# Kernel tuning notes

Hardware: AMD Instinct MI355X
Metric: run time of the kernel (lower is better)

Reference implementation:

```python
import jax, jax.numpy as jnp
import numpy as np

N, E = 100000, 1600000
D_IN, D_H, D_OUT = 128, 128, 64


def setup_inputs() -> dict:
    key = jax.random.key(0)
    ks = jax.random.split(key, 9)
    features = jax.random.normal(ks[0], (N, D_IN), dtype=jnp.float32)
    src = jax.random.randint(ks[1], (E,), 0, N, dtype=jnp.int32)
    dst = jax.random.randint(ks[2], (E,), 0, N, dtype=jnp.int32)
    # GraphConv weights (glorot-ish scale)
    W1 = jax.random.normal(ks[3], (D_IN, D_H), dtype=jnp.float32) * (1.0 / np.sqrt(D_IN))
    b1 = jnp.zeros((D_H,), dtype=jnp.float32)
    W2 = jax.random.normal(ks[4], (D_H, D_H), dtype=jnp.float32) * (1.0 / np.sqrt(D_H))
    b2 = jnp.zeros((D_H,), dtype=jnp.float32)
    W3 = jax.random.normal(ks[5], (D_H, D_OUT), dtype=jnp.float32) * (1.0 / np.sqrt(D_H))
    b3 = jnp.zeros((D_OUT,), dtype=jnp.float32)
    return {"features": features, "src": src, "dst": dst,
            "W1": W1, "b1": b1, "W2": W2, "b2": b2, "W3": W3, "b3": b3}


def reference(features, src, dst, W1, b1, W2, b2, W3, b3):
    n = features.shape[0]
    ones_e = jnp.ones(src.shape[0], dtype=features.dtype)
    # DGL GraphConv norm='both': degrees clamped to min 1
    out_deg = jnp.clip(jax.ops.segment_sum(ones_e, src, num_segments=n), 1.0)
    in_deg = jnp.clip(jax.ops.segment_sum(ones_e, dst, num_segments=n), 1.0)
    norm_src = out_deg ** -0.5  # [N]
    norm_dst = in_deg ** -0.5   # [N]

    def graph_conv(h, W, b, relu):
        h = h * norm_src[:, None]                                   # D_out^{-1/2} scale
        m = jax.ops.segment_sum(h[src], dst, num_segments=n)        # SpMM aggregate
        m = m * norm_dst[:, None]                                   # D_in^{-1/2} scale
        h = m @ W + b                                               # linear
        return jax.nn.relu(h) if relu else h

    # dropout is identity in eval mode (deterministic reference)
    h = graph_conv(features, W1, b1, True)
    h = graph_conv(h, W2, b2, True)
    h = graph_conv(h, W3, b3, False)
    return jax.nn.log_softmax(h, axis=1)
```

## Files before the change

### kernel.cpp

```cpp
#include <hip/hip_runtime.h>
#include <math.h>

#define D 128
#define DO 64

#define CHUNK_BITS 15
#define CHUNK_SZ   32768
#define HWORDS     (CHUNK_SZ/4)
#define NSLICE     64

typedef unsigned int uint32;
typedef short bf8s __attribute__((ext_vector_type(8)));
typedef float f32x16 __attribute__((ext_vector_type(16)));

__device__ __forceinline__ unsigned short f2bf(float f) {
    uint32 u = __float_as_uint(f);
    u += 0x7FFFu + ((u >> 16) & 1u);
    return (unsigned short)(u >> 16);
}
__device__ __forceinline__ float bf_lo(uint32 p) { return __uint_as_float(p << 16); }
__device__ __forceinline__ float bf_hi(uint32 p) { return __uint_as_float(p & 0xFFFF0000u); }
__device__ __forceinline__ void acc2(float4& a, uint2 q) {
    a.x += bf_lo(q.x); a.y += bf_hi(q.x);
    a.z += bf_lo(q.y); a.w += bf_hi(q.y);
}

__device__ __forceinline__ f32x16 mfma32(bf8s a, bf8s b, f32x16 c) {
    return __builtin_amdgcn_mfma_f32_32x32x16_bf16(a, b, c, 0, 0, 0);
}
#define ZERO16 {0.f,0.f,0.f,0.f,0.f,0.f,0.f,0.f,0.f,0.f,0.f,0.f,0.f,0.f,0.f,0.f}

__global__ void k_pack_w(const float* __restrict__ W1, const float* __restrict__ W2,
                         const float* __restrict__ W3,
                         unsigned short* __restrict__ P1, unsigned short* __restrict__ P2,
                         unsigned short* __restrict__ P3) {
    int t = blockIdx.x * 256 + threadIdx.x;
    const float* W; unsigned short* P; int slot, NCT, ncols;
    if (t < 2048)      { W = W1; P = P1; slot = t;        NCT = 4; ncols = 128; }
    else if (t < 4096) { W = W2; P = P2; slot = t - 2048; NCT = 4; ncols = 128; }
    else if (t < 5120) { W = W3; P = P3; slot = t - 4096; NCT = 2; ncols = 64;  }
    else return;
    int lane = slot & 63, rest = slot >> 6;
    int ct = rest % NCT, ks = rest / NCT;
    int k0 = ks * 16 + (lane >> 5) * 8;
    int colidx = ct * 32 + (lane & 31);
    unsigned u[4];
#pragma unroll
    for (int b = 0; b < 4; ++b) {
        unsigned lo = f2bf(W[(size_t)(k0 + 2 * b) * ncols + colidx]);
        unsigned hi = f2bf(W[(size_t)(k0 + 2 * b + 1) * ncols + colidx]);
        u[b] = lo | (hi << 16);
    }
    ((uint4*)P)[slot] = make_uint4(u[0], u[1], u[2], u[3]);
}

__global__ __launch_bounds__(256) void k_hist_gemm1(
    const int* __restrict__ src, const int* __restrict__ dst, int E,
    int NH, int NBg, int gemmPer,
    uint32* __restrict__ histS, uint32* __restrict__ histD,
    const float* __restrict__ F, const unsigned short* __restrict__ Wp1,
    unsigned short* __restrict__ T1, int N) {
    __shared__ __align__(16) char smemraw[64 * 132 * 4];
    const int tid = threadIdx.x;
    const int P = 1 + gemmPer;
    const int per = blockIdx.x / P;
    const int pos = blockIdx.x % P;

    if (pos == 0) {
        if (per >= 2 * NH) return;
        bool isS = per >= NH;
        int h = isS ? per - NH : per;
        int chunk = h / NSLICE, slice = h % NSLICE;
        const int* key = isS ? src : dst;
        uint32* hist = (uint32*)smemraw;
        for (int w = tid; w < HWORDS; w += 256) hist[w] = 0;
        __syncthreads();
        int base = chunk << CHUNK_BITS;
        const int nE4 = E >> 2;
        int lo = (int)(((long long)slice * nE4) / NSLICE);
        int hi = (int)(((long long)(slice + 1) * nE4) / NSLICE);
        for (int idx = lo + tid; idx < hi; idx += 256) {
            int4 k4 = ((const int4*)key)[idx];
            unsigned o;
            o = (unsigned)(k4.x - base); if (o < CHUNK_SZ) atomicAdd(&hist[o >> 2], 1u << ((o & 3) * 8));
            o = (unsigned)(k4.y - base); if (o < CHUNK_SZ) atomicAdd(&hist[o >> 2], 1u << ((o & 3) * 8));
            o = (unsigned)(k4.z - base); if (o < CHUNK_SZ) atomicAdd(&hist[o >> 2], 1u << ((o & 3) * 8));
            o = (unsigned)(k4.w - base); if (o < CHUNK_SZ) atomicAdd(&hist[o >> 2], 1u << ((o & 3) * 8));
        }
        if (slice == NSLICE - 1 && tid == 0) {
            for (int i = nE4 * 4; i < E; ++i) {
                unsigned o = (unsigned)(key[i] - base);
                if (o < CHUNK_SZ) atomicAdd(&hist[o >> 2], 1u << ((o & 3) * 8));
            }
        }
        __syncthreads();
        uint32* outp = (isS ? histS : histD) + (size_t)h * HWORDS;
        for (int w = tid; w < HWORDS; w += 256) outp[w] = hist[w];
        return;
    }
    int gid = per * gemmPer + (pos - 1);
    if (gid >= NBg) return;
    const int n0 = gid * 64;
    const float4* M4 = (const float4*)F;
#pragma unroll
    for (int it = 0; it < 8; ++it) {
        int id = it * 256 + tid;
        int nl = id >> 5, k4 = id & 31;
        float4 v = make_float4(0.f, 0.f, 0.f, 0.f);
        int n = n0 + nl;
        if (n < N) v = M4[(size_t)n * 32 + k4];
        ushort4 o;
        o.x = f2bf(v.x); o.y = f2bf(v.y); o.z = f2bf(v.z); o.w = f2bf(v.w);
        *(ushort4*)(smemraw + ((unsigned)(nl * 256 + k4 * 8) ^ ((nl & 15) << 4))) = o;
    }
    __syncthreads();
    const int wid = tid >> 6, wl = tid & 63;
    const int rt = wid >> 1, ctb = (wid & 1) * 2;
    const bf8s* Wp = (const bf8s*)Wp1;
    f32x16 acc0 = ZERO16, acc1 = ZERO16;
    const int arow = rt * 32 + (wl & 31);
    const unsigned axor = (unsigned)((arow & 15) << 4);
    const unsigned abase = (unsigned)(arow * 256 + (wl >> 5) * 16);
#pragma unroll
    for (int ks = 0; ks < 8; ++ks) {
        bf8s af = *(const bf8s*)(smemraw + ((abase + ks * 32) ^ axor));
        acc0 = mfma32(af, Wp[(ks * 4 + ctb) * 64 + wl], acc0);
        acc1 = mfma32(af, Wp[(ks * 4 + ctb + 1) * 64 + wl], acc1);
    }
    const int colb = wl & 31;
    const int rbase = rt * 32 + ((wl >> 5) << 2);
#pragma unroll
    for (int reg = 0; reg < 16; ++reg) {
        int n = n0 + (reg & 3) + 8 * (reg >> 2) + rbase;
        if (n < N) {
            T1[(size_t)n * 128 + ctb * 32 + colb] = f2bf(acc0[reg]);
            T1[(size_t)n * 128 + (ctb + 1) * 32 + colb] = f2bf(acc1[reg]);
        }
    }
}

__global__ void k_merge_norms(const uint32* __restrict__ histS, uint32* __restrict__ histD,
                              int* __restrict__ degi, float* __restrict__ ns,
                              float* __restrict__ nd, int N, int NCHUNK) {
    int w = blockIdx.x * 256 + threadIdx.x;
    if (w >= NCHUNK * HWORDS) return;
    int chunk = w / HWORDS, ww = w - chunk * HWORDS;
    int n0 = (chunk << CHUNK_BITS) + ww * 4;
    if (n0 >= N) return;
    size_t basehist = ((size_t)chunk * NSLICE) * HWORDS + ww;
    uint32 runD = 0, runS = 0;
#pragma unroll 4
    for (int s = 0; s < NSLICE; ++s) {
        size_t idx = basehist + (size_t)s * HWORDS;
        uint32 c = histD[idx];
        histD[idx] = runD;
        runD += c;
        runS += histS[idx];
    }
#pragma unroll
    for (int k = 0; k < 4; ++k) {
        int n = n0 + k;
        if (n < N) {
            int dcur = (int)((runD >> (k * 8)) & 0xFF);
            int ocur = (int)((runS >> (k * 8)) & 0xFF);
            degi[n] = dcur;
            ns[n] = rsqrtf((float)(ocur < 1 ? 1 : ocur));
            nd[n] = rsqrtf((float)(dcur < 1 ? 1 : dcur));
        }
    }
}

__global__ void k_scan_block(const int* __restrict__ cnt, int* __restrict__ rp,
                             int* __restrict__ bsum, int N) {
    __shared__ int sdat[256];
    int i = blockIdx.x * 256 + threadIdx.x;
    int v = (i < N) ? cnt[i] : 0;
    sdat[threadIdx.x] = v;
    __syncthreads();
    for (int off = 1; off < 256; off <<= 1) {
        int t = (threadIdx.x >= off) ? sdat[threadIdx.x - off] : 0;
        __syncthreads();
        sdat[threadIdx.x] += t;
        __syncthreads();
    }
    if (i < N) rp[i] = sdat[threadIdx.x] - v;
    if (threadIdx.x == 255) bsum[blockIdx.x] = sdat[255];
}

__global__ void k_scan_bsum(int* __restrict__ bsum, int NB) {
    __shared__ int sdat[512];
    int tid = threadIdx.x;
    int v = (tid < NB) ? bsum[tid] : 0;
    sdat[tid] = v;
    __syncthreads();
    for (int off = 1; off < 512; off <<= 1) {
        int t = (tid >= off) ? sdat[tid - off] : 0;
        __syncthreads();
        sdat[tid] += t;
        __syncthreads();
    }
    if (tid < NB) bsum[tid] = sdat[tid] - v;
}

__global__ void k_scan_add(int* __restrict__ rp, const int* __restrict__ bsum,
                           int N, int E, uint32* __restrict__ Az, uint32* __restrict__ Bz) {
    int i = blockIdx.x * 256 + threadIdx.x;
    if (i < N) rp[i] += bsum[i >> 8];
    if (i == N) rp[N] = E;
    if (i < 64) { Az[i] = 0; Bz[i] = 0; }
}

__global__ __launch_bounds__(256) void k_scatter_rescale(
    const int* __restrict__ src, const int* __restrict__ dst, int E,
    const uint32* __restrict__ histD, const int* __restrict__ rp,
    int* __restrict__ col, int NH,
    unsigned short* __restrict__ T1, const float* __restrict__ ns, int N) {
    __shared__ uint32 cnt[HWORDS];
    const int tid = threadIdx.x;
    if (blockIdx.x >= NH) {
        int i = (blockIdx.x - NH) * 256 + tid;
        if (i < N * 32) {
            float s = ns[i >> 5];
            uint2 q = ((uint2*)T1)[i];
            ushort4 o;
            o.x = f2bf(bf_lo(q.x) * s); o.y = f2bf(bf_hi(q.x) * s);
            o.z = f2bf(bf_lo(q.y) * s); o.w = f2bf(bf_hi(q.y) * s);
            ((uint2*)T1)[i] = *(uint2*)&o;
        }
        return;
    }
    int chunk = blockIdx.x / NSLICE, slice = blockIdx.x % NSLICE;
    const uint32* Pslice = histD + ((size_t)(chunk * NSLICE + slice)) * HWORDS;
    for (int w = tid; w < HWORDS; w += 256) cnt[w] = Pslice[w];
    __syncthreads();
    int base = chunk << CHUNK_BITS;
    const int nE4 = E >> 2;
    int lo = (int)(((long long)slice * nE4) / NSLICE);
    int hi = (int)(((long long)(slice + 1) * nE4) / NSLICE);
    for (int idx = lo + tid; idx < hi; idx += 256) {
        int4 s4 = ((const int4*)src)[idx];
        int4 d4 = ((const int4*)dst)[idx];
        unsigned o;
        o = (unsigned)(d4.x - base);
        if (o < CHUNK_SZ) {
            uint32 old = atomicAdd(&cnt[o >> 2], 1u << ((o & 3) * 8));
            col[rp[d4.x] + ((old >> ((o & 3) * 8)) & 0xFF)] = s4.x;
        }
        o = (unsigned)(d4.y - base);
        if (o < CHUNK_SZ) {
            uint32 old = atomicAdd(&cnt[o >> 2], 1u << ((o & 3) * 8));
            col[rp[d4.y] + ((old >> ((o & 3) * 8)) & 0xFF)] = s4.y;
        }
        o = (unsigned)(d4.z - base);
        if (o < CHUNK_SZ) {
            uint32 old = atomicAdd(&cnt[o >> 2], 1u << ((o & 3) * 8));
            col[rp[d4.z] + ((old >> ((o & 3) * 8)) & 0xFF)] = s4.z;
        }
        o = (unsigned)(d4.w - base);
        if (o < CHUNK_SZ) {
            uint32 old = atomicAdd(&cnt[o >> 2], 1u << ((o & 3) * 8));
            col[rp[d4.w] + ((old >> ((o & 3) * 8)) & 0xFF)] = s4.w;
        }
    }
    if (slice == NSLICE - 1 && tid == 0) {
        for (int i = nE4 * 4; i < E; ++i) {
            unsigned o = (unsigned)(dst[i] - base);
            if (o < CHUNK_SZ) {
                uint32 old = atomicAdd(&cnt[o >> 2], 1u << ((o & 3) * 8));
                col[rp[dst[i]] + ((old >> ((o & 3) * 8)) & 0xFF)] = src[i];
            }
        }
    }
}


#define SPMM_SH(K) int c##K = __shfl(cvec, j + K, 32);
#define SPMM_LD(K) uint2 q##K = T2[(((unsigned)c##K) << 5) + (unsigned)lane];
#define SPMM_AC(K) acc2(((K) & 1) ? a1 : a0, q##K);

__device__ __forceinline__ float4 spmm_gather_row(
    const uint2* __restrict__ T2, const int* __restrict__ col,
    int s, int e, int cvec, int lane, int N) {
    float4 a0 = make_float4(0.f, 0.f, 0.f, 0.f), a1 = a0;
    int base = s, rem = e - s;
#pragma unroll 1
    while (rem > 0) {
        int cnt = rem < 32 ? rem : 32;
        int padded = (cnt + 7) & ~7;
        int j = 0;
#pragma unroll 1
        for (; j + 16 <= padded; j += 16) {
            SPMM_SH(0) SPMM_SH(1) SPMM_SH(2) SPMM_SH(3)
            SPMM_SH(4) SPMM_SH(5) SPMM_SH(6) SPMM_SH(7)
            SPMM_SH(8) SPMM_SH(9) SPMM_SH(10) SPMM_SH(11)
            SPMM_SH(12) SPMM_SH(13) SPMM_SH(14) SPMM_SH(15)
            SPMM_LD(0) SPMM_LD(1) SPMM_LD(2) SPMM_LD(3)
            SPMM_LD(4) SPMM_LD(5) SPMM_LD(6) SPMM_LD(7)
            SPMM_LD(8) SPMM_LD(9) SPMM_LD(10) SPMM_LD(11)
            SPMM_LD(12) SPMM_LD(13) SPMM_LD(14) SPMM_LD(15)
            SPMM_AC(0) SPMM_AC(1) SPMM_AC(2) SPMM_AC(3)
            SPMM_AC(4) SPMM_AC(5) SPMM_AC(6) SPMM_AC(7)
            SPMM_AC(8) SPMM_AC(9) SPMM_AC(10) SPMM_AC(11)
            SPMM_AC(12) SPMM_AC(13) SPMM_AC(14) SPMM_AC(15)
        }
        if (j < padded) {
            SPMM_SH(0) SPMM_SH(1) SPMM_SH(2) SPMM_SH(3)
            SPMM_SH(4) SPMM_SH(5) SPMM_SH(6) SPMM_SH(7)
            SPMM_LD(0) SPMM_LD(1) SPMM_LD(2) SPMM_LD(3)
            SPMM_LD(4) SPMM_LD(5) SPMM_LD(6) SPMM_LD(7)
            SPMM_AC(0) SPMM_AC(1) SPMM_AC(2) SPMM_AC(3)
            SPMM_AC(4) SPMM_AC(5) SPMM_AC(6) SPMM_AC(7)
        }
        base += 32; rem -= 32;
        if (rem > 0) {
            int t = base + lane;
            cvec = (t < e) ? col[t] : N;
        }
    }
    float4 r;
    r.x = a0.x + a1.x; r.y = a0.y + a1.y;
    r.z = a0.z + a1.z; r.w = a0.w + a1.w;
    return r;
}

#define A64_SH(K) int c##K = __shfl(cvec, j + K, 32);
#define A64_LD(K) uint32 q##K = Y2[(((unsigned)c##K) << 5) + (unsigned)lane];
#define A64_AC(K) { if ((K) & 1) { lo1 += bf_lo(q##K); hi1 += bf_hi(q##K); } \
                    else         { lo0 += bf_lo(q##K); hi0 += bf_hi(q##K); } }

__device__ __forceinline__ float2 agg64_gather_row(
    const uint32* __restrict__ Y2, const int* __restrict__ col,
    int s, int e, int cvec, int lane, int N) {
    float lo0 = 0.f, hi0 = 0.f, lo1 = 0.f, hi1 = 0.f;
    int base = s, rem = e - s;
#pragma unroll 1
    while (rem > 0) {
        int cnt = rem < 32 ? rem : 32;
        int padded = (cnt + 7) & ~7;
        int j = 0;
#pragma unroll 1
        for (; j + 16 <= padded; j += 16) {
            A64_SH(0) A64_SH(1) A64_SH(2) A64_SH(3)
            A64_SH(4) A64_SH(5) A64_SH(6) A64_SH(7)
            A64_SH(8) A64_SH(9) A64_SH(10) A64_SH(11)
            A64_SH(12) A64_SH(13) A64_SH(14) A64_SH(15)
            A64_LD(0) A64_LD(1) A64_LD(2) A64_LD(3)
            A64_LD(4) A64_LD(5) A64_LD(6) A64_LD(7)
            A64_LD(8) A64_LD(9) A64_LD(10) A64_LD(11)
            A64_LD(12) A64_LD(13) A64_LD(14) A64_LD(15)
            A64_AC(0) A64_AC(1) A64_AC(2) A64_AC(3)
            A64_AC(4) A64_AC(5) A64_AC(6) A64_AC(7)
            A64_AC(8) A64_AC(9) A64_AC(10) A64_AC(11)
            A64_AC(12) A64_AC(13) A64_AC(14) A64_AC(15)
        }
        if (j < padded) {
            A64_SH(0) A64_SH(1) A64_SH(2) A64_SH(3)
            A64_SH(4) A64_SH(5) A64_SH(6) A64_SH(7)
            A64_LD(0) A64_LD(1) A64_LD(2) A64_LD(3)
            A64_LD(4) A64_LD(5) A64_LD(6) A64_LD(7)
            A64_AC(0) A64_AC(1) A64_AC(2) A64_AC(3)
            A64_AC(4) A64_AC(5) A64_AC(6) A64_AC(7)
        }
        base += 32; rem -= 32;
        if (rem > 0) {
            int t = base + lane;
            cvec = (t < e) ? col[t] : N;
        }
    }
    return make_float2(lo0 + lo1, hi0 + hi1);
}

template <int JOUT>
__global__ __launch_bounds__(256) void k_spmm_gemm(
    const unsigned short* __restrict__ T, const int* __restrict__ rp,
    const int* __restrict__ col, const float* __restrict__ ns,
    const float* __restrict__ nd, const float* __restrict__ bias,
    const unsigned short* __restrict__ Wpk, unsigned short* __restrict__ out, int N) {
    __shared__ __align__(16) char MsRaw[32 * 256];
    if (JOUT == 64 && blockIdx.x == 0 && threadIdx.x < 32) {
        ((uint32*)out)[(size_t)N * 32 + threadIdx.x] = 0;
    }
    const int n0 = blockIdx.x * 32;
    const int g = threadIdx.x >> 5;
    const int lane = threadIdx.x & 31;
    const uint2* T2 = (const uint2*)T;
    float4 bv = ((const float4*)bias)[lane];

    const int row0 = n0 + (g << 2);
    int rb = 0;
    {
        int idx = row0 + lane;
        if (idx > N) idx = N;
        if (lane < 5) rb = rp[idx];
    }
    int s0 = __shfl(rb, 0, 32), s1 = __shfl(rb, 1, 32), s2 = __shfl(rb, 2, 32),
        s3 = __shfl(rb, 3, 32), s4 = __shfl(rb, 4, 32);
    int cv0 = N, cv1 = N, cv2 = N, cv3 = N;
    { int t = s0 + lane; if (t < s1) cv0 = col[t]; }
    { int t = s1 + lane; if (t < s2) cv1 = col[t]; }
    { int t = s2 + lane; if (t < s3) cv2 = col[t]; }
    { int t = s3 + lane; if (t < s4) cv3 = col[t]; }

#define SPMM_ROW_EPI(RI, SS, EE, CV) { \
    float4 t = spmm_gather_row(T2, col, SS, EE, CV, lane, N); \
    int row = row0 + RI; \
    if (row < N) { \
        float sd = nd[row], sr = ns[row]; \
        ushort4 o; \
        o.x = f2bf(fmaxf(fmaf(t.x, sd, bv.x), 0.f) * sr); \
        o.y = f2bf(fmaxf(fmaf(t.y, sd, bv.y), 0.f) * sr); \
        o.z = f2bf(fmaxf(fmaf(t.z, sd, bv.z), 0.f) * sr); \
        o.w = f2bf(fmaxf(fmaf(t.w, sd, bv.w), 0.f) * sr); \
        int lr = row - n0; \
        *(ushort4*)(MsRaw + ((unsigned)(lr * 256 + lane * 8) ^ ((lr & 15) << 4))) = o; \
    } }

    SPMM_ROW_EPI(0, s0, s1, cv0)
    SPMM_ROW_EPI(1, s1, s2, cv1)
    SPMM_ROW_EPI(2, s2, s3, cv2)
    SPMM_ROW_EPI(3, s3, s4, cv3)
#undef SPMM_ROW_EPI

    __syncthreads();
    const int wid = threadIdx.x >> 6, wl = threadIdx.x & 63;
    const int NCT = (JOUT == 128) ? 4 : 2;
    if (JOUT == 128 || wid < 2) {
        const bf8s* Wp = (const bf8s*)Wpk;
        f32x16 acc = ZERO16;
        const int arow = wl & 31;
        const unsigned axor = (unsigned)((arow & 15) << 4);
        const unsigned abase = (unsigned)(arow * 256 + (wl >> 5) * 16);
#pragma unroll
        for (int ks = 0; ks < 8; ++ks) {
            bf8s af = *(const bf8s*)(MsRaw + ((abase + ks * 32) ^ axor));
            acc = mfma32(af, Wp[(ks * NCT + wid) * 64 + wl], acc);
        }
        const int colb = wid * 32 + (wl & 31);
        const int rb2 = (wl >> 5) << 2;
#pragma unroll
        for (int reg = 0; reg < 16; ++reg) {
            int n = n0 + (reg & 3) + 8 * (reg >> 2) + rb2;
            if (n < N) out[(size_t)n * JOUT + colb] = f2bf(acc[reg]);
        }
    }
}

__global__ __launch_bounds__(256) void k_agg64_lsm(
    const unsigned short* __restrict__ Y, const int* __restrict__ rp,
    const int* __restrict__ col, const float* __restrict__ nd,
    const float* __restrict__ b3, float* __restrict__ out, int N) {
    int row = blockIdx.x * 8 + (threadIdx.x >> 5);
    if (row >= N) return;
    int lane = threadIdx.x & 31;
    const uint32* Y2 = (const uint32*)Y;
    int s = rp[row], e = rp[row + 1];
    int cv;
    { int t = s + lane; cv = (t < e) ? col[t] : N; }
    float2 agg = agg64_gather_row(Y2, col, s, e, cv, lane, N);
    float sd = nd[row];
    float2 bb = ((const float2*)b3)[lane];
    float v0 = agg.x * sd + bb.x;
    float v1 = agg.y * sd + bb.y;
    float m = fmaxf(v0, v1);
#pragma unroll
    for (int o = 16; o; o >>= 1) m = fmaxf(m, __shfl_xor(m, o, 32));
    float ex = expf(v0 - m) + expf(v1 - m);
#pragma unroll
    for (int o = 16; o; o >>= 1) ex += __shfl_xor(ex, o, 32);
    float ls = m + logf(ex);
    ((float2*)out)[(size_t)row * 32 + lane] = make_float2(v0 - ls, v1 - ls);
}

extern "C" void kernel_launch(void* const* d_in, const int* in_sizes, int n_in,
                              void* d_out, int out_size, void* d_ws, size_t ws_size,
                              hipStream_t stream) {
    const float* features = (const float*)d_in[0];
    const int*   src      = (const int*)d_in[1];
    const int*   dst      = (const int*)d_in[2];
    const float* W1       = (const float*)d_in[3];
    const float* b1       = (const float*)d_in[4];
    const float* W2       = (const float*)d_in[5];
    const float* b2       = (const float*)d_in[6];
    const float* W3       = (const float*)d_in[7];
    const float* b3       = (const float*)d_in[8];
    float* out = (float*)d_out;

    const int N = in_sizes[0] / D;
    const int E = in_sizes[1];

    const int NCHUNK = (N + CHUNK_SZ - 1) >> CHUNK_BITS;
    const int NH = NCHUNK * NSLICE;

    char* p = (char*)d_ws;
    unsigned short* A = (unsigned short*)p; p += ((size_t)N + 1) * D * sizeof(unsigned short);
    unsigned short* B = (unsigned short*)p; p += ((size_t)N + 1) * D * sizeof(unsigned short);
    int* col    = (int*)p;   p += (size_t)E * sizeof(int);
    int* rp     = (int*)p;   p += ((size_t)N + 4) * sizeof(int);
    int* degi   = (int*)p;   p += (size_t)N * sizeof(int);
    float* ns   = (float*)p; p += (size_t)N * sizeof(float);
    float* nd   = (float*)p; p += (size_t)N * sizeof(float);
    int* bsum   = (int*)p;   p += 4096 * sizeof(int);
    uint32* histS = (uint32*)p; p += (size_t)NH * HWORDS * sizeof(uint32);
    uint32* histD = (uint32*)p; p += (size_t)NH * HWORDS * sizeof(uint32);
    unsigned short* Wp1 = (unsigned short*)p; p += 16384 * sizeof(unsigned short);
    unsigned short* Wp2 = (unsigned short*)p; p += 16384 * sizeof(unsigned short);
    unsigned short* Wp3 = (unsigned short*)p; p += 8192 * sizeof(unsigned short);

    const int gN  = (N + 255) / 256;
    const int NBg = (N + 63) / 64;
    const int periods = 2 * NH;
    const int gemmPer = (NBg + periods - 1) / periods;
    const int G1 = periods * (1 + gemmPer);

    k_pack_w<<<20, 256, 0, stream>>>(W1, W2, W3, Wp1, Wp2, Wp3);
    k_hist_gemm1<<<G1, 256, 0, stream>>>(src, dst, E, NH, NBg, gemmPer,
                                         histS, histD, features, Wp1, B, N);
    k_merge_norms<<<(NCHUNK * HWORDS + 255) / 256, 256, 0, stream>>>(
        histS, histD, degi, ns, nd, N, NCHUNK);
    k_scan_block<<<gN, 256, 0, stream>>>(degi, rp, bsum, N);
    k_scan_bsum<<<1, 512, 0, stream>>>(bsum, gN);
    k_scan_add<<<(N + 1 + 255) / 256, 256, 0, stream>>>(
        rp, bsum, N, E,
        (uint32*)(A + (size_t)N * D), (uint32*)(B + (size_t)N * D));
    const int RB = (N * 32 + 255) / 256;
    k_scatter_rescale<<<NH + RB, 256, 0, stream>>>(src, dst, E, histD, rp, col, NH,
                                                   B, ns, N);

    const int NBn32 = (N + 31) / 32;
    k_spmm_gemm<128><<<NBn32, 256, 0, stream>>>(B, rp, col, ns, nd, b1, Wp2, A, N);
    k_spmm_gemm<64><<<NBn32, 256, 0, stream>>>(A, rp, col, ns, nd, b2, Wp3, B, N);
    k_agg64_lsm<<<(N + 7) / 8, 256, 0, stream>>>(B, rp, col, nd, b3, out, N);
}
```

Measured before the change: 335.8 us.

## Gather rows with full 64-lane wavefronts and scalar col indices via readfirstlane

Replaces the half-wave (32-lane) row gather, which shuffled column indices across lanes, with full-wave processing. Each wavefront now handles one row at a time, loads column indices uniformly and broadcasts them with readfirstlane so the row address is scalar. Each lane fetches a narrower slice (4 bytes for 128-wide, 2 bytes for 64-wide), and the final log-softmax kernel now reduces over 64 lanes and covers 16 rows per block. The aim is fewer shuffles and scalar address arithmetic, but per-lane loads become smaller, which may lower memory efficiency. Rows are also processed one after another per wave, which cuts memory-level parallelism.

```diff
diff --git a/kernel.cpp b/kernel.cpp
--- a/kernel.cpp
+++ b/kernel.cpp
@@ -20,10 +20,6 @@
 }
 __device__ __forceinline__ float bf_lo(uint32 p) { return __uint_as_float(p << 16); }
 __device__ __forceinline__ float bf_hi(uint32 p) { return __uint_as_float(p & 0xFFFF0000u); }
-__device__ __forceinline__ void acc2(float4& a, uint2 q) {
-    a.x += bf_lo(q.x); a.y += bf_hi(q.x);
-    a.z += bf_lo(q.y); a.w += bf_hi(q.y);
-}
 
 __device__ __forceinline__ f32x16 mfma32(bf8s a, bf8s b, f32x16 c) {
     return __builtin_amdgcn_mfma_f32_32x32x16_bf16(a, b, c, 0, 0, 0);
@@ -274,101 +270,21 @@
 }
 
 
-#define SPMM_SH(K) int c##K = __shfl(cvec, j + K, 32);
-#define SPMM_LD(K) uint2 q##K = T2[(((unsigned)c##K) << 5) + (unsigned)lane];
-#define SPMM_AC(K) acc2(((K) & 1) ? a1 : a0, q##K);
-
-__device__ __forceinline__ float4 spmm_gather_row(
-    const uint2* __restrict__ T2, const int* __restrict__ col,
-    int s, int e, int cvec, int lane, int N) {
-    float4 a0 = make_float4(0.f, 0.f, 0.f, 0.f), a1 = a0;
-    int base = s, rem = e - s;
-#pragma unroll 1
-    while (rem > 0) {
-        int cnt = rem < 32 ? rem : 32;
-        int padded = (cnt + 7) & ~7;
-        int j = 0;
-#pragma unroll 1
-        for (; j + 16 <= padded; j += 16) {
-            SPMM_SH(0) SPMM_SH(1) SPMM_SH(2) SPMM_SH(3)
-            SPMM_SH(4) SPMM_SH(5) SPMM_SH(6) SPMM_SH(7)
-            SPMM_SH(8) SPMM_SH(9) SPMM_SH(10) SPMM_SH(11)
-            SPMM_SH(12) SPMM_SH(13) SPMM_SH(14) SPMM_SH(15)
-            SPMM_LD(0) SPMM_LD(1) SPMM_LD(2) SPMM_LD(3)
-            SPMM_LD(4) SPMM_LD(5) SPMM_LD(6) SPMM_LD(7)
-            SPMM_LD(8) SPMM_LD(9) SPMM_LD(10) SPMM_LD(11)
-            SPMM_LD(12) SPMM_LD(13) SPMM_LD(14) SPMM_LD(15)
-            SPMM_AC(0) SPMM_AC(1) SPMM_AC(2) SPMM_AC(3)
-            SPMM_AC(4) SPMM_AC(5) SPMM_AC(6) SPMM_AC(7)
-            SPMM_AC(8) SPMM_AC(9) SPMM_AC(10) SPMM_AC(11)
-            SPMM_AC(12) SPMM_AC(13) SPMM_AC(14) SPMM_AC(15)
-        }
-        if (j < padded) {
-            SPMM_SH(0) SPMM_SH(1) SPMM_SH(2) SPMM_SH(3)
-            SPMM_SH(4) SPMM_SH(5) SPMM_SH(6) SPMM_SH(7)
-            SPMM_LD(0) SPMM_LD(1) SPMM_LD(2) SPMM_LD(3)
-            SPMM_LD(4) SPMM_LD(5) SPMM_LD(6) SPMM_LD(7)
-            SPMM_AC(0) SPMM_AC(1) SPMM_AC(2) SPMM_AC(3)
-            SPMM_AC(4) SPMM_AC(5) SPMM_AC(6) SPMM_AC(7)
-        }
-        base += 32; rem -= 32;
-        if (rem > 0) {
-            int t = base + lane;
-            cvec = (t < e) ? col[t] : N;
-        }
-    }
-    float4 r;
-    r.x = a0.x + a1.x; r.y = a0.y + a1.y;
-    r.z = a0.z + a1.z; r.w = a0.w + a1.w;
-    return r;
-}
-
-#define A64_SH(K) int c##K = __shfl(cvec, j + K, 32);
-#define A64_LD(K) uint32 q##K = Y2[(((unsigned)c##K) << 5) + (unsigned)lane];
-#define A64_AC(K) { if ((K) & 1) { lo1 += bf_lo(q##K); hi1 += bf_hi(q##K); } \
-                    else         { lo0 += bf_lo(q##K); hi0 += bf_hi(q##K); } }
-
-__device__ __forceinline__ float2 agg64_gather_row(
-    const uint32* __restrict__ Y2, const int* __restrict__ col,
-    int s, int e, int cvec, int lane, int N) {
-    float lo0 = 0.f, hi0 = 0.f, lo1 = 0.f, hi1 = 0.f;
-    int base = s, rem = e - s;
-#pragma unroll 1
-    while (rem > 0) {
-        int cnt = rem < 32 ? rem : 32;
-        int padded = (cnt + 7) & ~7;
-        int j = 0;
-#pragma unroll 1
-        for (; j + 16 <= padded; j += 16) {
-            A64_SH(0) A64_SH(1) A64_SH(2) A64_SH(3)
-            A64_SH(4) A64_SH(5) A64_SH(6) A64_SH(7)
-            A64_SH(8) A64_SH(9) A64_SH(10) A64_SH(11)
-            A64_SH(12) A64_SH(13) A64_SH(14) A64_SH(15)
-            A64_LD(0) A64_LD(1) A64_LD(2) A64_LD(3)
-            A64_LD(4) A64_LD(5) A64_LD(6) A64_LD(7)
-            A64_LD(8) A64_LD(9) A64_LD(10) A64_LD(11)
-            A64_LD(12) A64_LD(13) A64_LD(14) A64_LD(15)
-            A64_AC(0) A64_AC(1) A64_AC(2) A64_AC(3)
-            A64_AC(4) A64_AC(5) A64_AC(6) A64_AC(7)
-            A64_AC(8) A64_AC(9) A64_AC(10) A64_AC(11)
-            A64_AC(12) A64_AC(13) A64_AC(14) A64_AC(15)
-        }
-        if (j < padded) {
-            A64_SH(0) A64_SH(1) A64_SH(2) A64_SH(3)
-            A64_SH(4) A64_SH(5) A64_SH(6) A64_SH(7)
-            A64_LD(0) A64_LD(1) A64_LD(2) A64_LD(3)
-            A64_LD(4) A64_LD(5) A64_LD(6) A64_LD(7)
-            A64_AC(0) A64_AC(1) A64_AC(2) A64_AC(3)
-            A64_AC(4) A64_AC(5) A64_AC(6) A64_AC(7)
-        }
-        base += 32; rem -= 32;
-        if (rem > 0) {
-            int t = base + lane;
-            cvec = (t < e) ? col[t] : N;
-        }
-    }
-    return make_float2(lo0 + lo1, hi0 + hi1);
-}
+#define RFL(x) __builtin_amdgcn_readfirstlane(x)
+
+#define SG_EDGE_U2(K) \
+    int jk##K = j + K; \
+    int jc##K = jk##K < e_ ? jk##K : e_ - 1; \
+    int cl##K = col[jc##K]; \
+    int ck##K = RFL(jk##K < e_ ? cl##K : N); \
+    uint32 q##K = *(const uint32*)((const char*)Tw + (((size_t)(unsigned)ck##K) << 8) + lb);
+
+#define SG_EDGE_U1(K) \
+    int jk##K = j + K; \
+    int jc##K = jk##K < e_ ? jk##K : e_ - 1; \
+    int cl##K = col[jc##K]; \
+    int ck##K = RFL(jk##K < e_ ? cl##K : N); \
+    uint32 u##K = (uint32)*(const unsigned short*)((const char*)Yw + (((size_t)(unsigned)ck##K) << 7) + lb);
 
 template <int JOUT>
 __global__ __launch_bounds__(256) void k_spmm_gemm(
@@ -381,62 +297,52 @@
         ((uint32*)out)[(size_t)N * 32 + threadIdx.x] = 0;
     }
     const int n0 = blockIdx.x * 32;
-    const int g = threadIdx.x >> 5;
-    const int lane = threadIdx.x & 31;
-    const uint2* T2 = (const uint2*)T;
-    float4 bv = ((const float4*)bias)[lane];
-
-    const int row0 = n0 + (g << 2);
-    int rb = 0;
-    {
-        int idx = row0 + lane;
-        if (idx > N) idx = N;
-        if (lane < 5) rb = rp[idx];
-    }
-    int s0 = __shfl(rb, 0, 32), s1 = __shfl(rb, 1, 32), s2 = __shfl(rb, 2, 32),
-        s3 = __shfl(rb, 3, 32), s4 = __shfl(rb, 4, 32);
-    int cv0 = N, cv1 = N, cv2 = N, cv3 = N;
-    { int t = s0 + lane; if (t < s1) cv0 = col[t]; }
-    { int t = s1 + lane; if (t < s2) cv1 = col[t]; }
-    { int t = s2 + lane; if (t < s3) cv2 = col[t]; }
-    { int t = s3 + lane; if (t < s4) cv3 = col[t]; }
-
-#define SPMM_ROW_EPI(RI, SS, EE, CV) { \
-    float4 t = spmm_gather_row(T2, col, SS, EE, CV, lane, N); \
-    int row = row0 + RI; \
-    if (row < N) { \
-        float sd = nd[row], sr = ns[row]; \
-        ushort4 o; \
-        o.x = f2bf(fmaxf(fmaf(t.x, sd, bv.x), 0.f) * sr); \
-        o.y = f2bf(fmaxf(fmaf(t.y, sd, bv.y), 0.f) * sr); \
-        o.z = f2bf(fmaxf(fmaf(t.z, sd, bv.z), 0.f) * sr); \
-        o.w = f2bf(fmaxf(fmaf(t.w, sd, bv.w), 0.f) * sr); \
-        int lr = row - n0; \
-        *(ushort4*)(MsRaw + ((unsigned)(lr * 256 + lane * 8) ^ ((lr & 15) << 4))) = o; \
-    } }
-
-    SPMM_ROW_EPI(0, s0, s1, cv0)
-    SPMM_ROW_EPI(1, s1, s2, cv1)
-    SPMM_ROW_EPI(2, s2, s3, cv2)
-    SPMM_ROW_EPI(3, s3, s4, cv3)
-#undef SPMM_ROW_EPI
+    const int wid = threadIdx.x >> 6;
+    const int wl = threadIdx.x & 63;
+    const uint32* Tw = (const uint32*)T;
+    const unsigned lb = (unsigned)(wl << 2);
+    float2 bb = ((const float2*)bias)[wl];
+
+#pragma unroll 1
+    for (int r = 0; r < 8; ++r) {
+        int row = n0 + wid * 8 + r;
+        int s_ = RFL(rp[row]);
+        int e_ = RFL(rp[row + 1]);
+        float ax0 = 0.f, ay0 = 0.f, ax1 = 0.f, ay1 = 0.f;
+#pragma unroll 1
+        for (int j = s_; j < e_; j += 8) {
+            SG_EDGE_U2(0) SG_EDGE_U2(1) SG_EDGE_U2(2) SG_EDGE_U2(3)
+            SG_EDGE_U2(4) SG_EDGE_U2(5) SG_EDGE_U2(6) SG_EDGE_U2(7)
+            ax0 += bf_lo(q0); ay0 += bf_hi(q0); ax1 += bf_lo(q1); ay1 += bf_hi(q1);
+            ax0 += bf_lo(q2); ay0 += bf_hi(q2); ax1 += bf_lo(q3); ay1 += bf_hi(q3);
+            ax0 += bf_lo(q4); ay0 += bf_hi(q4); ax1 += bf_lo(q5); ay1 += bf_hi(q5);
+            ax0 += bf_lo(q6); ay0 += bf_hi(q6); ax1 += bf_lo(q7); ay1 += bf_hi(q7);
+        }
+        float ax = ax0 + ax1, ay = ay0 + ay1;
+        float sd = nd[row], sr = ns[row];
+        float vx = fmaxf(fmaf(ax, sd, bb.x), 0.f) * sr;
+        float vy = fmaxf(fmaf(ay, sd, bb.y), 0.f) * sr;
+        uint32 o = (uint32)f2bf(vx) | ((uint32)f2bf(vy) << 16);
+        int lr = wid * 8 + r;
+        *(uint32*)(MsRaw + ((unsigned)(lr * 256 + wl * 4) ^ ((lr & 15) << 4))) = o;
+    }
 
     __syncthreads();
-    const int wid = threadIdx.x >> 6, wl = threadIdx.x & 63;
+    const int wl2 = threadIdx.x & 63;
     const int NCT = (JOUT == 128) ? 4 : 2;
     if (JOUT == 128 || wid < 2) {
         const bf8s* Wp = (const bf8s*)Wpk;
         f32x16 acc = ZERO16;
-        const int arow = wl & 31;
+        const int arow = wl2 & 31;
         const unsigned axor = (unsigned)((arow & 15) << 4);
-        const unsigned abase = (unsigned)(arow * 256 + (wl >> 5) * 16);
+        const unsigned abase = (unsigned)(arow * 256 + (wl2 >> 5) * 16);
 #pragma unroll
         for (int ks = 0; ks < 8; ++ks) {
             bf8s af = *(const bf8s*)(MsRaw + ((abase + ks * 32) ^ axor));
-            acc = mfma32(af, Wp[(ks * NCT + wid) * 64 + wl], acc);
-        }
-        const int colb = wid * 32 + (wl & 31);
-        const int rb2 = (wl >> 5) << 2;
+            acc = mfma32(af, Wp[(ks * NCT + wid) * 64 + wl2], acc);
+        }
+        const int colb = wid * 32 + (wl2 & 31);
+        const int rb2 = (wl2 >> 5) << 2;
 #pragma unroll
         for (int reg = 0; reg < 16; ++reg) {
             int n = n0 + (reg & 3) + 8 * (reg >> 2) + rb2;
@@ -449,26 +355,38 @@
     const unsigned short* __restrict__ Y, const int* __restrict__ rp,
     const int* __restrict__ col, const float* __restrict__ nd,
     const float* __restrict__ b3, float* __restrict__ out, int N) {
-    int row = blockIdx.x * 8 + (threadIdx.x >> 5);
-    if (row >= N) return;
-    int lane = threadIdx.x & 31;
-    const uint32* Y2 = (const uint32*)Y;
-    int s = rp[row], e = rp[row + 1];
-    int cv;
-    { int t = s + lane; cv = (t < e) ? col[t] : N; }
-    float2 agg = agg64_gather_row(Y2, col, s, e, cv, lane, N);
-    float sd = nd[row];
-    float2 bb = ((const float2*)b3)[lane];
-    float v0 = agg.x * sd + bb.x;
-    float v1 = agg.y * sd + bb.y;
-    float m = fmaxf(v0, v1);
-#pragma unroll
-    for (int o = 16; o; o >>= 1) m = fmaxf(m, __shfl_xor(m, o, 32));
-    float ex = expf(v0 - m) + expf(v1 - m);
-#pragma unroll
-    for (int o = 16; o; o >>= 1) ex += __shfl_xor(ex, o, 32);
-    float ls = m + logf(ex);
-    ((float2*)out)[(size_t)row * 32 + lane] = make_float2(v0 - ls, v1 - ls);
+    const int wid = threadIdx.x >> 6;
+    const int wl = threadIdx.x & 63;
+    const unsigned short* Yw = Y;
+    const unsigned lb = (unsigned)(wl << 1);
+    float bbv = b3[wl];
+#pragma unroll 1
+    for (int r = 0; r < 4; ++r) {
+        int row = blockIdx.x * 16 + wid * 4 + r;
+        if (row < N) {
+            int s_ = RFL(rp[row]);
+            int e_ = RFL(rp[row + 1]);
+            float a0 = 0.f, a1 = 0.f;
+#pragma unroll 1
+            for (int j = s_; j < e_; j += 8) {
+                SG_EDGE_U1(0) SG_EDGE_U1(1) SG_EDGE_U1(2) SG_EDGE_U1(3)
+                SG_EDGE_U1(4) SG_EDGE_U1(5) SG_EDGE_U1(6) SG_EDGE_U1(7)
+                a0 += __uint_as_float(u0 << 16); a1 += __uint_as_float(u1 << 16);
+                a0 += __uint_as_float(u2 << 16); a1 += __uint_as_float(u3 << 16);
+                a0 += __uint_as_float(u4 << 16); a1 += __uint_as_float(u5 << 16);
+                a0 += __uint_as_float(u6 << 16); a1 += __uint_as_float(u7 << 16);
+            }
+            float v = (a0 + a1) * nd[row] + bbv;
+            float m = v;
+#pragma unroll
+            for (int o = 32; o; o >>= 1) m = fmaxf(m, __shfl_xor(m, o, 64));
+            float ex = expf(v - m);
+#pragma unroll
+            for (int o = 32; o; o >>= 1) ex += __shfl_xor(ex, o, 64);
+            float ls = m + logf(ex);
+            out[(size_t)row * 64 + wl] = v - ls;
+        }
+    }
 }
 
 extern "C" void kernel_launch(void* const* d_in, const int* in_sizes, int n_in,
@@ -529,5 +447,5 @@
     const int NBn32 = (N + 31) / 32;
     k_spmm_gemm<128><<<NBn32, 256, 0, stream>>>(B, rp, col, ns, nd, b1, Wp2, A, N);
     k_spmm_gemm<64><<<NBn32, 256, 0, stream>>>(A, rp, col, ns, nd, b2, Wp3, B, N);
-    k_agg64_lsm<<<(N + 7) / 8, 256, 0, stream>>>(B, rp, col, nd, b3, out, N);
-}
+    k_agg64_lsm<<<(N + 15) / 16, 256, 0, stream>>>(B, rp, col, nd, b3, out, N);
+}
```

Result: slower. 368.2 us (+9.7%).
